# Kernel optimization log

Hardware: AMD Instinct MI355X
Metric: run time of the kernel (lower is better)

The kernel has to match this reference:

```python
import jax, jax.numpy as jnp
import numpy as np

D_MODEL = 1024
STATE_DIM = 16
BATCH = 32
SEQ = 2048


def setup_inputs() -> dict:
    key = jax.random.key(0)
    k_x, k_win, k_bin, k_wout, k_bout = jax.random.split(key, 5)
    proj_dim = 2 * D_MODEL + 3 * STATE_DIM
    x = jax.random.normal(k_x, (BATCH, SEQ, D_MODEL), dtype=jnp.float32)
    # Dense kernels (glorot-ish scale) and zero biases, as in fresh keras layers
    W_in = jax.random.normal(k_win, (D_MODEL, proj_dim), dtype=jnp.float32) * 0.02
    b_in = jnp.zeros((proj_dim,), dtype=jnp.float32)
    W_out = jax.random.normal(k_wout, (D_MODEL, D_MODEL), dtype=jnp.float32) * 0.02
    b_out = jnp.zeros((D_MODEL,), dtype=jnp.float32)
    # A_log init: -log([1..state_dim])
    A_log = -jnp.log(jnp.arange(1, STATE_DIM + 1, dtype=jnp.float32))
    return {"x": x, "W_in": W_in, "b_in": b_in, "A_log": A_log,
            "W_out": W_out, "b_out": b_out}


def _selective_scan(delta, A, B, C):
    # delta, B, C: [b, s, n]; A: [n]
    # state_t = exp(A * delta_t) * state_{t-1} + B_t ; y_t = sum(state_t * C_t)
    def step(state, inp):
        delta_t, B_t, C_t = inp  # each [b, n]
        state = jnp.exp(A * delta_t) * state + B_t
        y = jnp.sum(state * C_t, axis=-1)  # [b]
        return state, y

    b = delta.shape[0]
    init = jnp.zeros((b, A.shape[0]), dtype=delta.dtype)
    # scan over time: move seq axis to front -> [s, b, n]
    xs = (jnp.swapaxes(delta, 0, 1), jnp.swapaxes(B, 0, 1), jnp.swapaxes(C, 0, 1))
    _, ys = jax.lax.scan(step, init, xs)  # ys: [s, b]
    return jnp.swapaxes(ys, 0, 1)  # [b, s]


def reference(x, W_in, b_in, A_log, W_out, b_out):
    xz = jnp.einsum('bsd,dp->bsp', x, W_in) + b_in  # [b, s, 2*d + 3*n]
    d, n = D_MODEL, STATE_DIM
    xm = xz[..., :d]                     # unused by scan (matches original)
    z = xz[..., d:2 * d]                 # [b, s, d]
    Bm = xz[..., 2 * d:2 * d + n]        # [b, s, n]
    Cm = xz[..., 2 * d + n:2 * d + 2 * n]
    delta = jax.nn.softplus(xz[..., 2 * d + 2 * n:])  # [b, s, n]
    A = -jnp.exp(A_log)                  # [n]
    y = _selective_scan(delta, A, Bm, Cm)  # [b, s]
    y = y[..., None] * jax.nn.gelu(z, approximate=False)  # [b, s, d]
    return jnp.einsum('bsd,de->bse', y, W_out) + b_out
```

## Files before the change

kernel.cpp:

```cpp
#include <hip/hip_runtime.h>
#include <cstdint>

typedef float fx4 __attribute__((ext_vector_type(4)));
typedef short sx8 __attribute__((ext_vector_type(8)));
typedef short sx4 __attribute__((ext_vector_type(4)));

#define NSTATE 16
#define SEQ_LEN 2048
#define NBATCH 32
#define MROWS 65536
#define KDIM 1024
#define N1 1072
#define N1PAD 1152
#define BK 32
#define NSTEP (KDIM / BK)
#define TILE_SHORTS 4096
#define TSTRIDE (NSTEP * TILE_SHORTS)
#define RING 4
#define SLOT_SHORTS 8192

__device__ __forceinline__ short f2bf(float f) {
  unsigned u = __float_as_uint(f);
  u += 0x7FFFu + ((u >> 16) & 1u);
  return (short)(u >> 16);
}

__device__ __forceinline__ float gelu_exact(float x) {
  float ax = fabsf(x) * 0.70710678118654752f;
  float t = __builtin_amdgcn_rcpf(fmaf(0.3275911f, ax, 1.0f));
  float p = fmaf(1.061405429f, t, -1.453152027f);
  p = fmaf(p, t, 1.421413741f);
  p = fmaf(p, t, -0.284496736f);
  p = fmaf(p, t, 0.254829592f);
  p = p * t;
  float e = __expf(-ax * ax);
  float erfv = fmaf(-p, e, 1.0f);
  erfv = copysignf(erfv, x);
  return 0.5f * x * (1.0f + erfv);
}

#define GLOAD_LDS16(gp, lp)                                                          \
  __builtin_amdgcn_global_load_lds(                                                  \
      (const __attribute__((address_space(1))) unsigned int*)(gp),                   \
      (__attribute__((address_space(3))) unsigned int*)(lp), 16, 0, 0)

#define SBAR() do { __builtin_amdgcn_s_barrier(); asm volatile("" ::: "memory"); } while (0)

#define CT_STRIDE (TILE_SHORTS + 16)
__global__ void convert_pack_x(const float* __restrict__ x, short* __restrict__ xbp) {
  __shared__ short tbuf[4 * CT_STRIDE];
  const int t = threadIdx.x;
  const int p = blockIdx.x >> 3;
  const int kq = blockIdx.x & 7;
  const int l32 = t & 31;
  const int kt_local = l32 >> 3;
  const int q = (l32 & 7) >> 1;
  const int eo = (l32 & 1) * 4;
  const float* xb = x + ((long)p * 128) * KDIM + kq * 128 + l32 * 4;

#pragma unroll 4
  for (int i = 0; i < 16; ++i) {
    const int r = i * 8 + (t >> 5);
    fx4 v = *(const fx4*)(xb + (long)r * KDIM);
    sx4 o;
    o[0] = f2bf(v[0]); o[1] = f2bf(v[1]); o[2] = f2bf(v[2]); o[3] = f2bf(v[3]);
    const int phys = (q + (r >> 1)) & 3;
    *(sx4*)(tbuf + kt_local * CT_STRIDE + r * 32 + phys * 8 + eo) = o;
  }
  __syncthreads();

  const int w = t >> 6, l = t & 63;
  short* dst = xbp + (long)p * TSTRIDE + (long)(kq * 4 + w) * TILE_SHORTS;
  const short* src = tbuf + w * CT_STRIDE;
#pragma unroll
  for (int i = 0; i < 8; ++i)
    *(sx8*)(dst + i * 512 + l * 8) = *(const sx8*)(src + i * 512 + l * 8);
}

__global__ void transpose_w_kernel(const float* __restrict__ src, short* __restrict__ dst,
                                   int src_cols, int col_off, int valid_rows) {
  __shared__ float t[32][33];
  int j0 = blockIdx.x * 32;
  int k0 = blockIdx.y * 32;
  int c = threadIdx.x & 31;
  int r = threadIdx.x >> 5;
#pragma unroll
  for (int i = 0; i < 4; i++) {
    int k = k0 + r + i * 8;
    int j = j0 + c;
    float v = (j < valid_rows) ? src[(long)k * src_cols + col_off + j] : 0.f;
    t[r + i * 8][c] = v;
  }
  __syncthreads();
#pragma unroll
  for (int i = 0; i < 4; i++) {
    int n = j0 + r + i * 8;
    int k = k0 + c;
    int rr = n & 127;
    long addr = ((long)(n >> 7) * NSTEP + (k >> 5)) * TILE_SHORTS + rr * 32
              + ((((k >> 3) & 3) + ((rr >> 1) & 3)) & 3) * 8 + (k & 7);
    dst[addr] = f2bf(t[c][r + i * 8]);
  }
}

__device__ __forceinline__ void gemm_mainloop256(const short* __restrict__ Abase,
                                                 const short* __restrict__ Bbase,
                                                 short* lds, fx4 acc[4][4]) {
  const int tid = threadIdx.x;
  const int lane = tid & 63;
  const int wave = tid >> 6;
  const int wm = wave >> 2, wn = wave & 3;
  const int l15 = lane & 15, ks = lane >> 4;

#pragma unroll
  for (int i = 0; i < 4; i++)
#pragma unroll
    for (int j = 0; j < 4; j++) acc[i][j] = fx4{0.f, 0.f, 0.f, 0.f};

  short* AshR = lds;
  short* BshR = lds + RING * SLOT_SHORTS;
  const short* Asrc = Abase + (long)(tid >> 9) * TSTRIDE + (tid & 511) * 8;
  const short* Bsrc = Bbase + (long)(tid >> 9) * TSTRIDE + (tid & 511) * 8;
  const int dst = tid * 8;

  const int rslot = ((ks + (l15 >> 1)) & 3) * 8;
  const int aoff = (wm >> 1) * TILE_SHORTS + ((wm & 1) * 64 + l15) * 32 + rslot;
  const int boff = (wn >> 1) * TILE_SHORTS + ((wn & 1) * 64 + l15) * 32 + rslot;

#pragma unroll
  for (int s = 0; s < RING - 1; s++) {
    GLOAD_LDS16(Asrc + (long)s * TILE_SHORTS, AshR + s * SLOT_SHORTS + dst);
    GLOAD_LDS16(Bsrc + (long)s * TILE_SHORTS, BshR + s * SLOT_SHORTS + dst);
  }

  for (int s = 0; s < NSTEP; ++s) {
    const int rem = NSTEP - 1 - s;
    if (rem >= 2)      asm volatile("s_waitcnt vmcnt(4)" ::: "memory");
    else if (rem == 1) asm volatile("s_waitcnt vmcnt(2)" ::: "memory");
    else               asm volatile("s_waitcnt vmcnt(0)" ::: "memory");
    SBAR();

    if (s + 3 < NSTEP) {
      const int sl = (s + 3) & (RING - 1);
      GLOAD_LDS16(Asrc + (long)(s + 3) * TILE_SHORTS, AshR + sl * SLOT_SHORTS + dst);
      GLOAD_LDS16(Bsrc + (long)(s + 3) * TILE_SHORTS, BshR + sl * SLOT_SHORTS + dst);
    }

    const short* sa = AshR + (s & (RING - 1)) * SLOT_SHORTS + aoff;
    const short* sb = BshR + (s & (RING - 1)) * SLOT_SHORTS + boff;
    sx8 af[4], bfr[4];
#pragma unroll
    for (int i = 0; i < 4; i++) af[i] = *(const sx8*)(sa + i * 512);
#pragma unroll
    for (int j = 0; j < 4; j++) bfr[j] = *(const sx8*)(sb + j * 512);

    __builtin_amdgcn_s_setprio(1);
#pragma unroll
    for (int i = 0; i < 4; i++)
#pragma unroll
      for (int j = 0; j < 4; j++)
        acc[i][j] = __builtin_amdgcn_mfma_f32_16x16x32_bf16(af[i], bfr[j], acc[i][j], 0, 0, 0);
    __builtin_amdgcn_s_setprio(0);
  }
}

__global__ __launch_bounds__(1024, 1) void gemm1_kernel(
    const short* __restrict__ xbp, const short* __restrict__ Wt1p,
    const float* __restrict__ b_in, short* __restrict__ g) {
  extern __shared__ short lds[];
  const int bid = blockIdx.x;
  const int wgid = (bid & 7) * 128 + (bid >> 3);
  const int nt = wgid & 3;
  const int mt = wgid >> 2;
  fx4 acc[4][4];
  gemm_mainloop256(xbp + (long)(mt * 2) * TSTRIDE,
                   Wt1p + (long)(nt * 2) * TSTRIDE, lds, acc);

  const int lane = threadIdx.x & 63;
  const int wave = threadIdx.x >> 6;
  const int wm = wave >> 2, wn = wave & 3;
  const int m0 = mt * 256;
  const int n0 = nt * 256;

#pragma unroll
  for (int ni = 0; ni < 4; ni++) {
    int n = n0 + wn * 64 + ni * 16 + (lane & 15);
    float bias = b_in[1024 + n];
#pragma unroll
    for (int mi = 0; mi < 4; mi++) {
#pragma unroll
      for (int r = 0; r < 4; r++) {
        int m = m0 + wm * 64 + mi * 16 + (lane >> 4) * 4 + r;
        float v = acc[mi][ni][r] + bias;
        int rr = m & 127;
        long addr = ((long)(m >> 7) * NSTEP + (n >> 5)) * TILE_SHORTS + rr * 32
                  + ((((n >> 3) & 3) + ((rr >> 1) & 3)) & 3) * 8 + (n & 7);
        g[addr] = f2bf(gelu_exact(v));
      }
    }
  }
}

__global__ __launch_bounds__(256, 2) void gemm_bcd_kernel(
    const short* __restrict__ xbp, const short* __restrict__ Wt1p,
    const float* __restrict__ b_in, const float* __restrict__ A_log,
    float* __restrict__ Bb, float* __restrict__ Cb, float* __restrict__ ab) {
  __shared__ short Ash[3 * 4096] __attribute__((aligned(16)));
  __shared__ short Bsh[3 * 2048] __attribute__((aligned(16)));
  const int tid = threadIdx.x;
  const int lane = tid & 63, wave = tid >> 6;
  const int l15 = lane & 15, ks = lane >> 4;
  const int bid = blockIdx.x;
  const int mt = (bid & 7) * 64 + (bid >> 3);
  const short* Abase = xbp + (long)mt * TSTRIDE;
  const short* Bbase = Wt1p + (long)8 * TSTRIDE;

  fx4 acc[2][3];
#pragma unroll
  for (int i = 0; i < 2; i++)
#pragma unroll
    for (int j = 0; j < 3; j++) acc[i][j] = fx4{0.f, 0.f, 0.f, 0.f};

  const int rslot = ((ks + (l15 >> 1)) & 3) * 8;
  const int aofb = (wave * 32 + l15) * 32 + rslot;

#pragma unroll
  for (int s = 0; s < 2; s++) {
    GLOAD_LDS16(Abase + (long)s * TILE_SHORTS + tid * 8, Ash + s * 4096 + tid * 8);
    GLOAD_LDS16(Abase + (long)s * TILE_SHORTS + 2048 + tid * 8, Ash + s * 4096 + 2048 + tid * 8);
    GLOAD_LDS16(Bbase + (long)s * TILE_SHORTS + tid * 8, Bsh + s * 2048 + tid * 8);
  }

  for (int s = 0; s < NSTEP; ++s) {
    if (s < NSTEP - 1) asm volatile("s_waitcnt vmcnt(3)" ::: "memory");
    else               asm volatile("s_waitcnt vmcnt(0)" ::: "memory");
    SBAR();
    if (s + 2 < NSTEP) {
      const int sl = (s + 2) % 3;
      GLOAD_LDS16(Abase + (long)(s + 2) * TILE_SHORTS + tid * 8, Ash + sl * 4096 + tid * 8);
      GLOAD_LDS16(Abase + (long)(s + 2) * TILE_SHORTS + 2048 + tid * 8, Ash + sl * 4096 + 2048 + tid * 8);
      GLOAD_LDS16(Bbase + (long)(s + 2) * TILE_SHORTS + tid * 8, Bsh + sl * 2048 + tid * 8);
    }
    const short* sa = Ash + (s % 3) * 4096 + aofb;
    const short* sb = Bsh + (s % 3) * 2048;
    sx8 af[2], bfr[3];
#pragma unroll
    for (int i = 0; i < 2; i++) af[i] = *(const sx8*)(sa + i * 512);
#pragma unroll
    for (int j = 0; j < 3; j++) bfr[j] = *(const sx8*)(sb + (j * 16 + l15) * 32 + rslot);
#pragma unroll
    for (int i = 0; i < 2; i++)
#pragma unroll
      for (int j = 0; j < 3; j++)
        acc[i][j] = __builtin_amdgcn_mfma_f32_16x16x32_bf16(af[i], bfr[j], acc[i][j], 0, 0, 0);
  }

  const float biasB = b_in[2048 + l15];
  const float biasC = b_in[2064 + l15];
  const float biasD = b_in[2080 + l15];
  const float Ac = -expf(A_log[l15]);
#pragma unroll
  for (int mi = 0; mi < 2; mi++) {
#pragma unroll
    for (int r = 0; r < 4; r++) {
      int m = mt * 128 + wave * 32 + mi * 16 + (lane >> 4) * 4 + r;
      Bb[m * NSTATE + l15] = acc[mi][0][r] + biasB;
      Cb[m * NSTATE + l15] = acc[mi][1][r] + biasC;
      float v = acc[mi][2][r] + biasD;
      float dlt = (v > 20.f) ? v : log1pf(expf(v));
      ab[m * NSTATE + l15] = expf(Ac * dlt);
    }
  }
}

__global__ void scan_kernel(const float* __restrict__ ab, const float* __restrict__ Bb,
                            const float* __restrict__ Cb, float* __restrict__ y) {
  __shared__ float Ash[16][17], Bsh[16][17];
  const int b = blockIdx.x;
  const int tid = threadIdx.x;
  const int seg = tid >> 4, ch = tid & 15;
  const long base = ((long)b * SEQ_LEN + seg * 128) * NSTATE + ch;
  const float* pa = ab + base;
  const float* pb = Bb + base;
  const float* pc = Cb + base;

  float A = 1.f, Bc = 0.f;
  for (int i0 = 0; i0 < 128; i0 += 8) {
    float av[8], bv[8];
#pragma unroll
    for (int u = 0; u < 8; u++) { av[u] = pa[(i0 + u) * NSTATE]; bv[u] = pb[(i0 + u) * NSTATE]; }
#pragma unroll
    for (int u = 0; u < 8; u++) { Bc = fmaf(av[u], Bc, bv[u]); A *= av[u]; }
  }
  Ash[seg][ch] = A; Bsh[seg][ch] = Bc;
  __syncthreads();

  if (tid < 16) {
    float s = 0.f;
    for (int sg = 0; sg < 16; ++sg) {
      float nxt = fmaf(Ash[sg][tid], s, Bsh[sg][tid]);
      Bsh[sg][tid] = s;
      s = nxt;
    }
  }
  __syncthreads();

  float s = Bsh[seg][ch];
  float* py = y + (long)b * SEQ_LEN + seg * 128;
  for (int i0 = 0; i0 < 128; i0 += 8) {
    float av[8], bv[8], cv[8];
#pragma unroll
    for (int u = 0; u < 8; u++) {
      av[u] = pa[(i0 + u) * NSTATE];
      bv[u] = pb[(i0 + u) * NSTATE];
      cv[u] = pc[(i0 + u) * NSTATE];
    }
#pragma unroll
    for (int u = 0; u < 8; u++) {
      s = fmaf(av[u], s, bv[u]);
      float p = s * cv[u];
      p += __shfl_xor(p, 1);
      p += __shfl_xor(p, 2);
      p += __shfl_xor(p, 4);
      p += __shfl_xor(p, 8);
      if (ch == 0) py[i0 + u] = p;
    }
  }
}

__global__ __launch_bounds__(1024, 1) void gemm2_kernel(
    const short* __restrict__ g, const short* __restrict__ Wt2p,
    const float* __restrict__ y, const float* __restrict__ b_out,
    float* __restrict__ out) {
  extern __shared__ short lds[];
  const int bid = blockIdx.x;
  const int wgid = (bid & 7) * 128 + (bid >> 3);
  const int nt = wgid & 3;
  const int mt = wgid >> 2;
  fx4 acc[4][4];
  gemm_mainloop256(g + (long)(mt * 2) * TSTRIDE,
                   Wt2p + (long)(nt * 2) * TSTRIDE, lds, acc);

  const int lane = threadIdx.x & 63;
  const int wave = threadIdx.x >> 6;
  const int wm = wave >> 2, wn = wave & 3;
  const int m0 = mt * 256;
  const int n0 = nt * 256;

#pragma unroll
  for (int mi = 0; mi < 4; mi++) {
#pragma unroll
    for (int r = 0; r < 4; r++) {
      int m = m0 + wm * 64 + mi * 16 + (lane >> 4) * 4 + r;
      float ym = y[m];
#pragma unroll
      for (int ni = 0; ni < 4; ni++) {
        int n = n0 + wn * 64 + ni * 16 + (lane & 15);
        out[(long)m * 1024 + n] = fmaf(ym, acc[mi][ni][r], b_out[n]);
      }
    }
  }
}

extern "C" void kernel_launch(void* const* d_in, const int* in_sizes, int n_in,
                              void* d_out, int out_size, void* d_ws, size_t ws_size,
                              hipStream_t stream) {
  const float* x     = (const float*)d_in[0];
  const float* W_in  = (const float*)d_in[1];
  const float* b_in  = (const float*)d_in[2];
  const float* A_log = (const float*)d_in[3];
  const float* W_out = (const float*)d_in[4];
  const float* b_out = (const float*)d_in[5];
  float* out = (float*)d_out;

  char* ws = (char*)d_ws;
  short* xbp = (short*)ws;  ws += (size_t)MROWS * KDIM * 2;
  short* g   = (short*)ws;  ws += (size_t)MROWS * KDIM * 2;
  short* Wt1p = (short*)ws; ws += (size_t)N1PAD * KDIM * 2;
  short* Wt2p = (short*)ws; ws += (size_t)KDIM * KDIM * 2;
  float* Bb = (float*)ws;  ws += (size_t)MROWS * NSTATE * 4;
  float* Cb = (float*)ws;  ws += (size_t)MROWS * NSTATE * 4;
  float* ab = (float*)ws;  ws += (size_t)MROWS * NSTATE * 4;
  float* y  = (float*)ws;  ws += (size_t)MROWS * 4;

  const int ldsBytes = 2 * RING * SLOT_SHORTS * 2;

  convert_pack_x<<<4096, 256, 0, stream>>>(x, xbp);
  transpose_w_kernel<<<dim3(N1PAD / 32, 32), 256, 0, stream>>>(W_in, Wt1p, 2096, 1024, N1);
  transpose_w_kernel<<<dim3(32, 32), 256, 0, stream>>>(W_out, Wt2p, 1024, 0, 1024);
  gemm_bcd_kernel<<<512, 256, 0, stream>>>(xbp, Wt1p, b_in, A_log, Bb, Cb, ab);
  scan_kernel<<<NBATCH, 256, 0, stream>>>(ab, Bb, Cb, y);
  gemm1_kernel<<<1024, 1024, ldsBytes, stream>>>(xbp, Wt1p, b_in, g);
  gemm2_kernel<<<1024, 1024, ldsBytes, stream>>>(g, Wt2p, y, b_out, out);
}
```

Baseline: 472.4 us.

## Fuse B/C/delta projection into x conversion kernel with atomic split-K reduction

Folds the small B/C/delta GEMM into the x-to-bf16 pack kernel. Each block computes a partial 128-row by 48-column product over its 128-wide K slice, using the freshly converted tile already in LDS, and accumulates it into zeroed fp32 buffers with atomicAdd. This removes the separate gemm_bcd pass that re-read all of xbp. The bias, softplus and exp are moved into the scan kernel, which now recomputes them in both of its passes. It also drops the s_setprio hints in the main GEMM loop and adds a memset. The cost is atomic traffic, which is 8-way per element.

```diff
diff --git a/kernel.cpp b/kernel.cpp
--- a/kernel.cpp
+++ b/kernel.cpp
@@ -47,8 +47,12 @@
 #define SBAR() do { __builtin_amdgcn_s_barrier(); asm volatile("" ::: "memory"); } while (0)
 
 #define CT_STRIDE (TILE_SHORTS + 16)
-__global__ void convert_pack_x(const float* __restrict__ x, short* __restrict__ xbp) {
+__global__ __launch_bounds__(256) void convert_pack_x(
+    const float* __restrict__ x, const short* __restrict__ Wt1p,
+    short* __restrict__ xbp, float* __restrict__ Braw,
+    float* __restrict__ Craw, float* __restrict__ Draw) {
   __shared__ short tbuf[4 * CT_STRIDE];
+  __shared__ short wbuf[4 * 2048];
   const int t = threadIdx.x;
   const int p = blockIdx.x >> 3;
   const int kq = blockIdx.x & 7;
@@ -58,6 +62,11 @@
   const int eo = (l32 & 1) * 4;
   const float* xb = x + ((long)p * 128) * KDIM + kq * 128 + l32 * 4;
 
+  const short* Wb = Wt1p + (long)8 * TSTRIDE + (long)(kq * 4) * TILE_SHORTS;
+#pragma unroll
+  for (int c = 0; c < 4; ++c)
+    GLOAD_LDS16(Wb + (long)c * TILE_SHORTS + t * 8, wbuf + c * 2048 + t * 8);
+
 #pragma unroll 4
   for (int i = 0; i < 16; ++i) {
     const int r = i * 8 + (t >> 5);
@@ -70,11 +79,47 @@
   __syncthreads();
 
   const int w = t >> 6, l = t & 63;
-  short* dst = xbp + (long)p * TSTRIDE + (long)(kq * 4 + w) * TILE_SHORTS;
-  const short* src = tbuf + w * CT_STRIDE;
-#pragma unroll
-  for (int i = 0; i < 8; ++i)
-    *(sx8*)(dst + i * 512 + l * 8) = *(const sx8*)(src + i * 512 + l * 8);
+  {
+    short* dst = xbp + (long)p * TSTRIDE + (long)(kq * 4 + w) * TILE_SHORTS;
+    const short* src = tbuf + w * CT_STRIDE;
+#pragma unroll
+    for (int i = 0; i < 8; ++i)
+      *(sx8*)(dst + i * 512 + l * 8) = *(const sx8*)(src + i * 512 + l * 8);
+  }
+
+  const int l15 = l & 15, ks = l >> 4;
+  const int rslot = ((ks + (l15 >> 1)) & 3) * 8;
+  fx4 acc[2][3];
+#pragma unroll
+  for (int i = 0; i < 2; i++)
+#pragma unroll
+    for (int j = 0; j < 3; j++) acc[i][j] = fx4{0.f, 0.f, 0.f, 0.f};
+#pragma unroll
+  for (int kt = 0; kt < 4; ++kt) {
+    const short* sa = tbuf + kt * CT_STRIDE;
+    const short* sb = wbuf + kt * 2048;
+    sx8 af[2], bf[3];
+#pragma unroll
+    for (int mi = 0; mi < 2; mi++) af[mi] = *(const sx8*)(sa + (w * 32 + mi * 16 + l15) * 32 + rslot);
+#pragma unroll
+    for (int j = 0; j < 3; j++) bf[j] = *(const sx8*)(sb + (j * 16 + l15) * 32 + rslot);
+#pragma unroll
+    for (int mi = 0; mi < 2; mi++)
+#pragma unroll
+      for (int j = 0; j < 3; j++)
+        acc[mi][j] = __builtin_amdgcn_mfma_f32_16x16x32_bf16(af[mi], bf[j], acc[mi][j], 0, 0, 0);
+  }
+  const long mbase = (long)p * 128 + w * 32;
+#pragma unroll
+  for (int mi = 0; mi < 2; mi++) {
+#pragma unroll
+    for (int r = 0; r < 4; r++) {
+      long m = mbase + mi * 16 + (l >> 4) * 4 + r;
+      atomicAdd(&Braw[m * NSTATE + l15], acc[mi][0][r]);
+      atomicAdd(&Craw[m * NSTATE + l15], acc[mi][1][r]);
+      atomicAdd(&Draw[m * NSTATE + l15], acc[mi][2][r]);
+    }
+  }
 }
 
 __global__ void transpose_w_kernel(const float* __restrict__ src, short* __restrict__ dst,
@@ -154,13 +199,11 @@
 #pragma unroll
     for (int j = 0; j < 4; j++) bfr[j] = *(const sx8*)(sb + j * 512);
 
-    __builtin_amdgcn_s_setprio(1);
 #pragma unroll
     for (int i = 0; i < 4; i++)
 #pragma unroll
       for (int j = 0; j < 4; j++)
         acc[i][j] = __builtin_amdgcn_mfma_f32_16x16x32_bf16(af[i], bfr[j], acc[i][j], 0, 0, 0);
-    __builtin_amdgcn_s_setprio(0);
   }
 }
 
@@ -201,94 +244,32 @@
   }
 }
 
-__global__ __launch_bounds__(256, 2) void gemm_bcd_kernel(
-    const short* __restrict__ xbp, const short* __restrict__ Wt1p,
-    const float* __restrict__ b_in, const float* __restrict__ A_log,
-    float* __restrict__ Bb, float* __restrict__ Cb, float* __restrict__ ab) {
-  __shared__ short Ash[3 * 4096] __attribute__((aligned(16)));
-  __shared__ short Bsh[3 * 2048] __attribute__((aligned(16)));
-  const int tid = threadIdx.x;
-  const int lane = tid & 63, wave = tid >> 6;
-  const int l15 = lane & 15, ks = lane >> 4;
-  const int bid = blockIdx.x;
-  const int mt = (bid & 7) * 64 + (bid >> 3);
-  const short* Abase = xbp + (long)mt * TSTRIDE;
-  const short* Bbase = Wt1p + (long)8 * TSTRIDE;
-
-  fx4 acc[2][3];
-#pragma unroll
-  for (int i = 0; i < 2; i++)
-#pragma unroll
-    for (int j = 0; j < 3; j++) acc[i][j] = fx4{0.f, 0.f, 0.f, 0.f};
-
-  const int rslot = ((ks + (l15 >> 1)) & 3) * 8;
-  const int aofb = (wave * 32 + l15) * 32 + rslot;
-
-#pragma unroll
-  for (int s = 0; s < 2; s++) {
-    GLOAD_LDS16(Abase + (long)s * TILE_SHORTS + tid * 8, Ash + s * 4096 + tid * 8);
-    GLOAD_LDS16(Abase + (long)s * TILE_SHORTS + 2048 + tid * 8, Ash + s * 4096 + 2048 + tid * 8);
-    GLOAD_LDS16(Bbase + (long)s * TILE_SHORTS + tid * 8, Bsh + s * 2048 + tid * 8);
-  }
-
-  for (int s = 0; s < NSTEP; ++s) {
-    if (s < NSTEP - 1) asm volatile("s_waitcnt vmcnt(3)" ::: "memory");
-    else               asm volatile("s_waitcnt vmcnt(0)" ::: "memory");
-    SBAR();
-    if (s + 2 < NSTEP) {
-      const int sl = (s + 2) % 3;
-      GLOAD_LDS16(Abase + (long)(s + 2) * TILE_SHORTS + tid * 8, Ash + sl * 4096 + tid * 8);
-      GLOAD_LDS16(Abase + (long)(s + 2) * TILE_SHORTS + 2048 + tid * 8, Ash + sl * 4096 + 2048 + tid * 8);
-      GLOAD_LDS16(Bbase + (long)(s + 2) * TILE_SHORTS + tid * 8, Bsh + sl * 2048 + tid * 8);
-    }
-    const short* sa = Ash + (s % 3) * 4096 + aofb;
-    const short* sb = Bsh + (s % 3) * 2048;
-    sx8 af[2], bfr[3];
-#pragma unroll
-    for (int i = 0; i < 2; i++) af[i] = *(const sx8*)(sa + i * 512);
-#pragma unroll
-    for (int j = 0; j < 3; j++) bfr[j] = *(const sx8*)(sb + (j * 16 + l15) * 32 + rslot);
-#pragma unroll
-    for (int i = 0; i < 2; i++)
-#pragma unroll
-      for (int j = 0; j < 3; j++)
-        acc[i][j] = __builtin_amdgcn_mfma_f32_16x16x32_bf16(af[i], bfr[j], acc[i][j], 0, 0, 0);
-  }
-
-  const float biasB = b_in[2048 + l15];
-  const float biasC = b_in[2064 + l15];
-  const float biasD = b_in[2080 + l15];
-  const float Ac = -expf(A_log[l15]);
-#pragma unroll
-  for (int mi = 0; mi < 2; mi++) {
-#pragma unroll
-    for (int r = 0; r < 4; r++) {
-      int m = mt * 128 + wave * 32 + mi * 16 + (lane >> 4) * 4 + r;
-      Bb[m * NSTATE + l15] = acc[mi][0][r] + biasB;
-      Cb[m * NSTATE + l15] = acc[mi][1][r] + biasC;
-      float v = acc[mi][2][r] + biasD;
-      float dlt = (v > 20.f) ? v : log1pf(expf(v));
-      ab[m * NSTATE + l15] = expf(Ac * dlt);
-    }
-  }
-}
-
-__global__ void scan_kernel(const float* __restrict__ ab, const float* __restrict__ Bb,
-                            const float* __restrict__ Cb, float* __restrict__ y) {
+__global__ void scan_kernel(const float* __restrict__ Braw, const float* __restrict__ Craw,
+                            const float* __restrict__ Draw, const float* __restrict__ b_in,
+                            const float* __restrict__ A_log, float* __restrict__ y) {
   __shared__ float Ash[16][17], Bsh[16][17];
   const int b = blockIdx.x;
   const int tid = threadIdx.x;
   const int seg = tid >> 4, ch = tid & 15;
   const long base = ((long)b * SEQ_LEN + seg * 128) * NSTATE + ch;
-  const float* pa = ab + base;
-  const float* pb = Bb + base;
-  const float* pc = Cb + base;
+  const float* pB = Braw + base;
+  const float* pC = Craw + base;
+  const float* pD = Draw + base;
+  const float biasB = b_in[2048 + ch];
+  const float biasC = b_in[2064 + ch];
+  const float biasD = b_in[2080 + ch];
+  const float Ac = -expf(A_log[ch]);
 
   float A = 1.f, Bc = 0.f;
   for (int i0 = 0; i0 < 128; i0 += 8) {
     float av[8], bv[8];
 #pragma unroll
-    for (int u = 0; u < 8; u++) { av[u] = pa[(i0 + u) * NSTATE]; bv[u] = pb[(i0 + u) * NSTATE]; }
+    for (int u = 0; u < 8; u++) {
+      float d = pD[(i0 + u) * NSTATE] + biasD;
+      float dlt = (d > 20.f) ? d : log1pf(expf(d));
+      av[u] = expf(Ac * dlt);
+      bv[u] = pB[(i0 + u) * NSTATE] + biasB;
+    }
 #pragma unroll
     for (int u = 0; u < 8; u++) { Bc = fmaf(av[u], Bc, bv[u]); A *= av[u]; }
   }
@@ -311,9 +292,11 @@
     float av[8], bv[8], cv[8];
 #pragma unroll
     for (int u = 0; u < 8; u++) {
-      av[u] = pa[(i0 + u) * NSTATE];
-      bv[u] = pb[(i0 + u) * NSTATE];
-      cv[u] = pc[(i0 + u) * NSTATE];
+      float d = pD[(i0 + u) * NSTATE] + biasD;
+      float dlt = (d > 20.f) ? d : log1pf(expf(d));
+      av[u] = expf(Ac * dlt);
+      bv[u] = pB[(i0 + u) * NSTATE] + biasB;
+      cv[u] = pC[(i0 + u) * NSTATE] + biasC;
     }
 #pragma unroll
     for (int u = 0; u < 8; u++) {
@@ -378,18 +361,18 @@
   short* g   = (short*)ws;  ws += (size_t)MROWS * KDIM * 2;
   short* Wt1p = (short*)ws; ws += (size_t)N1PAD * KDIM * 2;
   short* Wt2p = (short*)ws; ws += (size_t)KDIM * KDIM * 2;
-  float* Bb = (float*)ws;  ws += (size_t)MROWS * NSTATE * 4;
-  float* Cb = (float*)ws;  ws += (size_t)MROWS * NSTATE * 4;
-  float* ab = (float*)ws;  ws += (size_t)MROWS * NSTATE * 4;
+  float* Braw = (float*)ws; ws += (size_t)MROWS * NSTATE * 4;
+  float* Craw = (float*)ws; ws += (size_t)MROWS * NSTATE * 4;
+  float* Draw = (float*)ws; ws += (size_t)MROWS * NSTATE * 4;
   float* y  = (float*)ws;  ws += (size_t)MROWS * 4;
 
   const int ldsBytes = 2 * RING * SLOT_SHORTS * 2;
 
-  convert_pack_x<<<4096, 256, 0, stream>>>(x, xbp);
+  hipMemsetAsync(Braw, 0, (size_t)3 * MROWS * NSTATE * 4, stream);
   transpose_w_kernel<<<dim3(N1PAD / 32, 32), 256, 0, stream>>>(W_in, Wt1p, 2096, 1024, N1);
   transpose_w_kernel<<<dim3(32, 32), 256, 0, stream>>>(W_out, Wt2p, 1024, 0, 1024);
-  gemm_bcd_kernel<<<512, 256, 0, stream>>>(xbp, Wt1p, b_in, A_log, Bb, Cb, ab);
-  scan_kernel<<<NBATCH, 256, 0, stream>>>(ab, Bb, Cb, y);
+  convert_pack_x<<<4096, 256, 0, stream>>>(x, Wt1p, xbp, Braw, Craw, Draw);
+  scan_kernel<<<NBATCH, 256, 0, stream>>>(Braw, Craw, Draw, b_in, A_log, y);
   gemm1_kernel<<<1024, 1024, ldsBytes, stream>>>(xbp, Wt1p, b_in, g);
   gemm2_kernel<<<1024, 1024, ldsBytes, stream>>>(g, Wt2p, y, b_out, out);
 }
```

Measured after the change: 612.2 us. 1.3x slower.
